# Performance work log

Measured on AMD Instinct MI355X. Metric: run time of the kernel, lower is better.

## Reference

```python
import jax, jax.numpy as jnp
import numpy as np

N, E, F_IN, H, C = 50000, 800000, 128, 64, 10

def setup_inputs() -> dict:
    key = jax.random.key(0)
    ks = jax.random.split(key, 8)
    x = jax.random.normal(ks[0], (N, F_IN), dtype=jnp.float32)
    edge_index = jax.random.randint(ks[1], (2, E), 0, N, dtype=jnp.int32)
    edge_weight = jax.random.uniform(ks[2], (E,), dtype=jnp.float32)
    W1 = jax.random.normal(ks[3], (H, F_IN), dtype=jnp.float32) * 0.05
    W2 = jax.random.normal(ks[4], (H, H), dtype=jnp.float32) * 0.05
    W3 = jax.random.normal(ks[5], (C, H), dtype=jnp.float32) * 0.05
    b1 = jnp.zeros((H,), jnp.float32)
    b2 = jnp.zeros((H,), jnp.float32)
    b3 = jnp.zeros((C,), jnp.float32)
    return {"x": x, "edge_index": edge_index, "edge_weight": edge_weight,
            "W1": W1, "b1": b1, "W2": W2, "b2": b2, "W3": W3, "b3": b3}

def reference(x, edge_index, edge_weight, W1, b1, W2, b2, W3, b3):
    n = x.shape[0]
    row, col = edge_index[0], edge_index[1]
    # GCN symmetric normalization (add_self_loops=False): deg from edge weights on col
    deg = jax.ops.segment_sum(edge_weight, col, num_segments=n)  # [N]
    dinv = jnp.where(deg > 0, jax.lax.rsqrt(deg), 0.0)
    norm = dinv[row] * edge_weight * dinv[col]  # [E]

    def gcn_layer(h, W, b):
        h = h @ W.T                               # linear transform [N, out]
        msg = h[row] * norm[:, None]              # gather + scale   [E, out]
        agg = jax.ops.segment_sum(msg, col, num_segments=n)  # scatter-add [N, out]
        return agg + b

    h = gcn_layer(x, W1, b1)
    h = gcn_layer(h, W2, b2)
    logits = gcn_layer(h, W3, b3)
    soft = jax.nn.softmax(logits, axis=1)
    return logits, soft
```

## Files before the change

### kernel.cpp

```cpp
#include <hip/hip_runtime.h>
#include <hip/hip_fp16.h>

#define N_NODES 50000
#define N_EDGES 800000
#define F_IN    128
#define H_DIM   64
#define C_DIM   10
#define CPAD    16
#define CAP     48
#define BLOCK   256
#define BIN_NODES 256
#define NBINS   196
#define STRIDE  4480
#define E_BLK   4096
#define ABLOCKS 196
#define DGB     (N_NODES / 16)
#define WB      ((N_NODES * 64) / 256)
#define POISON  ((int)0xAAAAAAAA)

__device__ __forceinline__ int unbase(int v) {
    return ((unsigned)v < 65536u) ? v : v - POISON;
}

__device__ __forceinline__ int   prow(unsigned v) { return (int)(v >> 16); }
__device__ __forceinline__ float pw(unsigned v)   {
    return __half2float(__ushort_as_half((unsigned short)(v & 0xFFFFu)));
}

__global__ __launch_bounds__(256) void k_binA(const int* __restrict__ rows,
                                              const int* __restrict__ cols,
                                              const float* __restrict__ ew,
                                              const float* __restrict__ W1,
                                              const float* __restrict__ b1,
                                              const float* __restrict__ W2,
                                              const float* __restrict__ b2,
                                              const float* __restrict__ W3,
                                              int* __restrict__ bucketCnt,
                                              unsigned* __restrict__ regionA,
                                              unsigned short* __restrict__ regionC,
                                              float* __restrict__ T2g,
                                              float* __restrict__ v1g,
                                              float* __restrict__ v2g) {
    const int tid = threadIdx.x;
    if (blockIdx.x < ABLOCKS) {
        __shared__ unsigned       sA[E_BLK];
        __shared__ unsigned short sC[E_BLK];
        __shared__ int hcnt[NBINS];
        __shared__ int lbase[NBINS];
        __shared__ int gb[NBINS];
        for (int i = tid; i < NBINS; i += BLOCK) hcnt[i] = 0;
        __syncthreads();

        const int e0 = blockIdx.x * E_BLK;
        unsigned rw[16];
        unsigned cl[16];
#pragma unroll
        for (int j = 0; j < 16; ++j) {
            int e = e0 + j * BLOCK + tid;
            if (e < N_EDGES) {
                int   c = cols[e];
                int   r = rows[e];
                float w = ew[e];
                rw[j] = ((unsigned)r << 16) | (unsigned)__half_as_ushort(__float2half(w));
                int lr = atomicAdd(&hcnt[c >> 8], 1);
                cl[j] = (unsigned)c | ((unsigned)lr << 16);
            } else {
                cl[j] = 0xFFFFFFFFu;
            }
        }
        __syncthreads();

        if (tid < 64) {
            int run = 0;
            for (int base = 0; base < NBINS; base += 64) {
                int i = base + tid;
                int v = (i < NBINS) ? hcnt[i] : 0;
                int s = v;
#pragma unroll
                for (int off = 1; off < 64; off <<= 1) {
                    int t = __shfl_up(s, off);
                    if (tid >= off) s += t;
                }
                if (i < NBINS) lbase[i] = run + s - v;
                run += __shfl(s, 63);
            }
        }
        __syncthreads();

#pragma unroll
        for (int j = 0; j < 16; ++j) {
            if (cl[j] != 0xFFFFFFFFu) {
                int c  = (int)(cl[j] & 0xFFFFu);
                int lr = (int)(cl[j] >> 16);
                int pos = lbase[c >> 8] + lr;
                sA[pos] = rw[j];
                sC[pos] = (unsigned short)c;
            }
        }
        if (tid < NBINS) gb[tid] = unbase(atomicAdd(&bucketCnt[tid], hcnt[tid]));
        __syncthreads();

        const int total = lbase[NBINS - 1] + hcnt[NBINS - 1];
        for (int i = tid; i < total; i += BLOCK) {
            int c = sC[i];
            int b = c >> 8;
            int gpos = gb[b] + (i - lbase[b]);
            if (gpos < STRIDE) {
                size_t p = (size_t)b * STRIDE + gpos;
                regionA[p] = sA[i];
                regionC[p] = (unsigned short)c;
            }
        }
        return;
    }

    __shared__ float u[C_DIM * H_DIM];
    for (int idx = tid; idx < C_DIM * H_DIM; idx += BLOCK) {
        int c = idx >> 6, j = idx & 63;
        float a = 0.f;
#pragma unroll
        for (int k = 0; k < H_DIM; ++k) a += W3[c * H_DIM + k] * W2[k * H_DIM + j];
        u[idx] = a;
    }
    __syncthreads();
    for (int idx = tid; idx < C_DIM * F_IN; idx += BLOCK) {
        int c = idx >> 7, f = idx & 127;
        float a = 0.f;
#pragma unroll
        for (int k = 0; k < H_DIM; ++k) a += u[c * H_DIM + k] * W1[k * F_IN + f];
        T2g[idx] = a;
    }
    if (tid < C_DIM) {
        float a = 0.f, b = 0.f;
#pragma unroll
        for (int k = 0; k < H_DIM; ++k) {
            a += u[tid * H_DIM + k] * b1[k];
            b += W3[tid * H_DIM + k] * b2[k];
        }
        v1g[tid] = a;
        v2g[tid] = b;
    }
}

__global__ __launch_bounds__(256) void k_binB(const int* __restrict__ bucketCnt,
                                              const unsigned* __restrict__ regionA,
                                              const unsigned short* __restrict__ regionC,
                                              int* __restrict__ cnt,
                                              float* __restrict__ dinv,
                                              unsigned* __restrict__ edata) {
    __shared__ unsigned sdata[BIN_NODES * CAP];
    __shared__ int   lcnt[BIN_NODES];
    __shared__ float wsum[BIN_NODES];
    const int tid = threadIdx.x;
    const int b   = blockIdx.x;
    if (tid < BIN_NODES) { lcnt[tid] = 0; wsum[tid] = 0.f; }
    __syncthreads();

    int tot = unbase(bucketCnt[b]);
    if (tot > STRIDE) tot = STRIDE;
    const size_t segBase = (size_t)b * STRIDE;
    for (int i = tid; i < tot; i += BLOCK) {
        unsigned e = regionA[segBase + i];
        int nl = (int)regionC[segBase + i] - b * BIN_NODES;
        int r = atomicAdd(&lcnt[nl], 1);
        if (r < CAP) sdata[nl * CAP + r] = e;
        atomicAdd(&wsum[nl], pw(e));
    }
    __syncthreads();

    const int n0 = b * BIN_NODES;
    const int nvalid = min(N_NODES - n0, BIN_NODES);
    int4* dst = reinterpret_cast<int4*>(edata + (size_t)n0 * CAP);
    const int4* src = reinterpret_cast<const int4*>(sdata);
    const int nvec = nvalid * CAP / 4;
    for (int i = tid; i < nvec; i += BLOCK) dst[i] = src[i];
    if (tid < nvalid) {
        int n = n0 + tid;
        cnt[n] = min(lcnt[tid], CAP);
        float d = wsum[tid];
        dinv[n] = d > 0.f ? rsqrtf(d) : 0.f;
    }
}

__global__ __launch_bounds__(256) void k_dg(const float* __restrict__ x,
                                            const float* __restrict__ T2g,
                                            const float* __restrict__ dinv,
                                            __half* __restrict__ bufA) {
    __shared__ float ts[16 * 132];
    __shared__ float xs[16][132];
    const int tid = threadIdx.x;
    const int n0 = blockIdx.x * 16;

    for (int i = tid; i < 16 * F_IN; i += BLOCK) {
        int c = i >> 7;
        ts[c * 132 + (i & 127)] = (c < C_DIM) ? T2g[i] : 0.f;
    }
    for (int i = tid; i < 16 * 32; i += BLOCK) {
        int ln = i >> 5, f4 = i & 31;
        float4 v = reinterpret_cast<const float4*>(x)[(n0 + ln) * 32 + f4];
        *reinterpret_cast<float4*>(&xs[ln][f4 * 4]) = v;
    }
    __syncthreads();

    const int g = tid >> 4;
    const int c = tid & 15;
    const int n = n0 + g;
    const float di = dinv[n];

    const float4* tsv = reinterpret_cast<const float4*>(&ts[c * 132]);
    const float4* xv  = reinterpret_cast<const float4*>(&xs[g][0]);
    float a = 0.f;
#pragma unroll 8
    for (int f4 = 0; f4 < 32; ++f4) {
        float4 xx = xv[f4], tt = tsv[f4];
        a += xx.x * tt.x + xx.y * tt.y + xx.z * tt.z + xx.w * tt.w;
    }
    float outv = (c < C_DIM) ? a * di : (c == 10 ? di : 0.f);
    bufA[n * CPAD + c] = __float2half(outv);
}

__global__ __launch_bounds__(256) void k_gather(const int* __restrict__ cnt,
                                                const unsigned* __restrict__ edata,
                                                const float* __restrict__ dinv,
                                                const __half* __restrict__ zin,
                                                __half* __restrict__ zout) {
    int n = (blockIdx.x * 256 + threadIdx.x) >> 6;
    if (n >= N_NODES) return;
    int lane = threadIdx.x & 63;
    int sub = lane >> 4, c = lane & 15;
    int count = cnt[n];
    if (count > CAP) count = CAP;
    int beg = n * CAP, end = beg + count;
    float acc = 0.f;
    int k = beg + sub;
    for (; k + 12 < end; k += 16) {
        unsigned e0 = edata[k];
        unsigned e1 = edata[k + 4];
        unsigned e2 = edata[k + 8];
        unsigned e3 = edata[k + 12];
        float v0 = __half2float(zin[prow(e0) * CPAD + c]);
        float v1 = __half2float(zin[prow(e1) * CPAD + c]);
        float v2 = __half2float(zin[prow(e2) * CPAD + c]);
        float v3 = __half2float(zin[prow(e3) * CPAD + c]);
        acc += pw(e0) * v0;
        acc += pw(e1) * v1;
        acc += pw(e2) * v2;
        acc += pw(e3) * v3;
    }
    for (; k < end; k += 4) {
        unsigned ed = edata[k];
        acc += pw(ed) * __half2float(zin[prow(ed) * CPAD + c]);
    }
    acc += __shfl_xor(acc, 32);
    acc += __shfl_xor(acc, 16);
    if (lane < 16) {
        float di = dinv[n];
        zout[n * CPAD + lane] = __float2half(acc * di * di);
    }
}

__global__ __launch_bounds__(256) void k_final(const int* __restrict__ cnt,
                                               const unsigned* __restrict__ edata,
                                               const float* __restrict__ dinv,
                                               const __half* __restrict__ zin,
                                               const __half* __restrict__ s1buf,
                                               const float* __restrict__ v1,
                                               const float* __restrict__ v2,
                                               const float* __restrict__ b3,
                                               float* __restrict__ logits,
                                               float* __restrict__ soft) {
    int n = (blockIdx.x * 256 + threadIdx.x) >> 6;
    if (n >= N_NODES) return;
    int lane = threadIdx.x & 63;
    int sub = lane >> 4, c = lane & 15;
    int count = cnt[n];
    if (count > CAP) count = CAP;
    int beg = n * CAP, end = beg + count;
    float acc = 0.f;
    int k = beg + sub;
    for (; k + 12 < end; k += 16) {
        unsigned e0 = edata[k];
        unsigned e1 = edata[k + 4];
        unsigned e2 = edata[k + 8];
        unsigned e3 = edata[k + 12];
        float w0 = __half2float(zin[prow(e0) * CPAD + c]);
        float w1 = __half2float(zin[prow(e1) * CPAD + c]);
        float w2 = __half2float(zin[prow(e2) * CPAD + c]);
        float w3 = __half2float(zin[prow(e3) * CPAD + c]);
        acc += pw(e0) * w0;
        acc += pw(e1) * w1;
        acc += pw(e2) * w2;
        acc += pw(e3) * w3;
    }
    for (; k < end; k += 4) {
        unsigned ed = edata[k];
        acc += pw(ed) * __half2float(zin[prow(ed) * CPAD + c]);
    }
    acc += __shfl_xor(acc, 32);
    acc += __shfl_xor(acc, 16);

    float di = dinv[n];
    float r  = di > 0.f ? 1.0f / di : 0.f;
    float a1 = __half2float(s1buf[n * CPAD + 10]) * r;
    float a2 = __half2float(zin[n * CPAD + 10]) * r;
    float l = (c < C_DIM) ? di * acc + a2 * v1[c] + a1 * v2[c] + b3[c] : -1e30f;
    float m = l;
#pragma unroll
    for (int d = 8; d >= 1; d >>= 1) m = fmaxf(m, __shfl_xor(m, d));
    float ev = (c < C_DIM) ? __expf(l - m) : 0.f;
    float s = ev;
#pragma unroll
    for (int d = 8; d >= 1; d >>= 1) s += __shfl_xor(s, d);
    if (lane < C_DIM) {
        logits[n * C_DIM + lane] = l;
        soft[n * C_DIM + lane]   = ev / s;
    }
}

extern "C" void kernel_launch(void* const* d_in, const int* in_sizes, int n_in,
                              void* d_out, int out_size, void* d_ws, size_t ws_size,
                              hipStream_t stream) {
    const float* x  = (const float*)d_in[0];
    const int*   ei = (const int*)d_in[1];
    const float* ew = (const float*)d_in[2];
    const float* W1 = (const float*)d_in[3];
    const float* b1 = (const float*)d_in[4];
    const float* W2 = (const float*)d_in[5];
    const float* b2 = (const float*)d_in[6];
    const float* W3 = (const float*)d_in[7];
    const float* b3 = (const float*)d_in[8];
    const int* rows = ei;
    const int* cols = ei + N_EDGES;

    char* ws = (char*)d_ws;
    size_t off = 0;
    auto alloc = [&](size_t bytes) { void* q = ws + off; off += (bytes + 15) & ~size_t(15); return q; };

    int*            cnt       = (int*)            alloc((size_t)N_NODES * 4);
    float*          dinv      = (float*)          alloc((size_t)N_NODES * 4);
    __half*         bufA      = (__half*)         alloc((size_t)N_NODES * CPAD * 2);
    __half*         bufB      = (__half*)         alloc((size_t)N_NODES * CPAD * 2);
    float*          T2g       = (float*)          alloc(C_DIM * F_IN * 4);
    float*          v1        = (float*)          alloc(64);
    float*          v2        = (float*)          alloc(64);
    int*            bucketCnt = (int*)            alloc(NBINS * 4);
    unsigned*       regionA   = (unsigned*)       alloc((size_t)NBINS * STRIDE * 4);
    unsigned short* regionC   = (unsigned short*) alloc((size_t)NBINS * STRIDE * 2);
    unsigned*       edata     = (unsigned*)       alloc((size_t)N_NODES * CAP * 4);

    float* logits = (float*)d_out;
    float* soft   = logits + N_NODES * C_DIM;

    k_binA<<<ABLOCKS + 1, 256, 0, stream>>>(rows, cols, ew, W1, b1, W2, b2, W3,
                                            bucketCnt, regionA, regionC, T2g, v1, v2);
    k_binB<<<NBINS, 256, 0, stream>>>(bucketCnt, regionA, regionC, cnt, dinv, edata);
    k_dg<<<DGB, 256, 0, stream>>>(x, T2g, dinv, bufA);
    k_gather<<<WB, 256, 0, stream>>>(cnt, edata, dinv, bufA, bufB);
    k_gather<<<WB, 256, 0, stream>>>(cnt, edata, dinv, bufB, bufA);
    k_final<<<WB, 256, 0, stream>>>(cnt, edata, dinv, bufA, bufB, v1, v2, b3,
                                    logits, soft);
}
```

Baseline: 177.8 us.

## Pack dinv and padded count into float2 meta, zero-pad edge lists, halve binning block

Per-node dinv and edge count are merged into one float2 array so each gather thread makes a single metadata load. Edge lists are zero-padded to a multiple of 16 inside binB, which lets the gather and final kernels run a fixed unrolled loop of up to 3 iterations with no tail loop. The binning kernel now covers 2048 edges per block, doubling the block count and halving per-thread register arrays. In exchange, padded zero-weight entries gather row 0, adding wasted loads, and binB gains an extra sync.

New measurement: 166.7 us. 6.2% less time.

```diff
diff --git a/kernel.cpp b/kernel.cpp
--- a/kernel.cpp
+++ b/kernel.cpp
@@ -12,8 +12,8 @@
 #define BIN_NODES 256
 #define NBINS   196
 #define STRIDE  4480
-#define E_BLK   4096
-#define ABLOCKS 196
+#define E_BLK   2048
+#define ABLOCKS ((N_EDGES + E_BLK - 1) / E_BLK)
 #define DGB     (N_NODES / 16)
 #define WB      ((N_NODES * 64) / 256)
 #define POISON  ((int)0xAAAAAAAA)
@@ -52,10 +52,10 @@
         __syncthreads();
 
         const int e0 = blockIdx.x * E_BLK;
-        unsigned rw[16];
-        unsigned cl[16];
-#pragma unroll
-        for (int j = 0; j < 16; ++j) {
+        unsigned rw[8];
+        unsigned cl[8];
+#pragma unroll
+        for (int j = 0; j < 8; ++j) {
             int e = e0 + j * BLOCK + tid;
             if (e < N_EDGES) {
                 int   c = cols[e];
@@ -88,7 +88,7 @@
         __syncthreads();
 
 #pragma unroll
-        for (int j = 0; j < 16; ++j) {
+        for (int j = 0; j < 8; ++j) {
             if (cl[j] != 0xFFFFFFFFu) {
                 int c  = (int)(cl[j] & 0xFFFFu);
                 int lr = (int)(cl[j] >> 16);
@@ -145,8 +145,7 @@
 __global__ __launch_bounds__(256) void k_binB(const int* __restrict__ bucketCnt,
                                               const unsigned* __restrict__ regionA,
                                               const unsigned short* __restrict__ regionC,
-                                              int* __restrict__ cnt,
-                                              float* __restrict__ dinv,
+                                              float2* __restrict__ meta,
                                               unsigned* __restrict__ edata) {
     __shared__ unsigned sdata[BIN_NODES * CAP];
     __shared__ int   lcnt[BIN_NODES];
@@ -170,21 +169,25 @@
 
     const int n0 = b * BIN_NODES;
     const int nvalid = min(N_NODES - n0, BIN_NODES);
+    if (tid < nvalid) {
+        int c0 = min(lcnt[tid], CAP);
+        int cp = (c0 + 15) & ~15;
+        if (cp > CAP) cp = CAP;
+        for (int r = c0; r < cp; ++r) sdata[tid * CAP + r] = 0u;
+        float d = wsum[tid];
+        meta[n0 + tid] = make_float2(d > 0.f ? rsqrtf(d) : 0.f, (float)cp);
+    }
+    __syncthreads();
+
     int4* dst = reinterpret_cast<int4*>(edata + (size_t)n0 * CAP);
     const int4* src = reinterpret_cast<const int4*>(sdata);
     const int nvec = nvalid * CAP / 4;
     for (int i = tid; i < nvec; i += BLOCK) dst[i] = src[i];
-    if (tid < nvalid) {
-        int n = n0 + tid;
-        cnt[n] = min(lcnt[tid], CAP);
-        float d = wsum[tid];
-        dinv[n] = d > 0.f ? rsqrtf(d) : 0.f;
-    }
 }
 
 __global__ __launch_bounds__(256) void k_dg(const float* __restrict__ x,
                                             const float* __restrict__ T2g,
-                                            const float* __restrict__ dinv,
+                                            const float2* __restrict__ meta,
                                             __half* __restrict__ bufA) {
     __shared__ float ts[16 * 132];
     __shared__ float xs[16][132];
@@ -205,7 +208,7 @@
     const int g = tid >> 4;
     const int c = tid & 15;
     const int n = n0 + g;
-    const float di = dinv[n];
+    const float di = meta[n].x;
 
     const float4* tsv = reinterpret_cast<const float4*>(&ts[c * 132]);
     const float4* xv  = reinterpret_cast<const float4*>(&xs[g][0]);
@@ -219,49 +222,40 @@
     bufA[n * CPAD + c] = __float2half(outv);
 }
 
-__global__ __launch_bounds__(256) void k_gather(const int* __restrict__ cnt,
+__global__ __launch_bounds__(256) void k_gather(const float2* __restrict__ meta,
                                                 const unsigned* __restrict__ edata,
-                                                const float* __restrict__ dinv,
                                                 const __half* __restrict__ zin,
                                                 __half* __restrict__ zout) {
     int n = (blockIdx.x * 256 + threadIdx.x) >> 6;
     if (n >= N_NODES) return;
     int lane = threadIdx.x & 63;
     int sub = lane >> 4, c = lane & 15;
-    int count = cnt[n];
-    if (count > CAP) count = CAP;
-    int beg = n * CAP, end = beg + count;
+    float2 m = meta[n];
+    float di = m.x;
+    int iters = ((int)m.y) >> 4;
+    int base = n * CAP + sub;
     float acc = 0.f;
-    int k = beg + sub;
-    for (; k + 12 < end; k += 16) {
-        unsigned e0 = edata[k];
-        unsigned e1 = edata[k + 4];
-        unsigned e2 = edata[k + 8];
-        unsigned e3 = edata[k + 12];
-        float v0 = __half2float(zin[prow(e0) * CPAD + c]);
-        float v1 = __half2float(zin[prow(e1) * CPAD + c]);
-        float v2 = __half2float(zin[prow(e2) * CPAD + c]);
-        float v3 = __half2float(zin[prow(e3) * CPAD + c]);
-        acc += pw(e0) * v0;
-        acc += pw(e1) * v1;
-        acc += pw(e2) * v2;
-        acc += pw(e3) * v3;
-    }
-    for (; k < end; k += 4) {
-        unsigned ed = edata[k];
-        acc += pw(ed) * __half2float(zin[prow(ed) * CPAD + c]);
+#pragma unroll
+    for (int i = 0; i < 3; ++i) {
+        if (i < iters) {
+            int k = base + i * 16;
+            unsigned e0 = edata[k];
+            unsigned e1 = edata[k + 4];
+            unsigned e2 = edata[k + 8];
+            unsigned e3 = edata[k + 12];
+            acc += pw(e0) * __half2float(zin[prow(e0) * CPAD + c]);
+            acc += pw(e1) * __half2float(zin[prow(e1) * CPAD + c]);
+            acc += pw(e2) * __half2float(zin[prow(e2) * CPAD + c]);
+            acc += pw(e3) * __half2float(zin[prow(e3) * CPAD + c]);
+        }
     }
     acc += __shfl_xor(acc, 32);
     acc += __shfl_xor(acc, 16);
-    if (lane < 16) {
-        float di = dinv[n];
-        zout[n * CPAD + lane] = __float2half(acc * di * di);
-    }
-}
-
-__global__ __launch_bounds__(256) void k_final(const int* __restrict__ cnt,
+    if (lane < 16) zout[n * CPAD + lane] = __float2half(acc * di * di);
+}
+
+__global__ __launch_bounds__(256) void k_final(const float2* __restrict__ meta,
                                                const unsigned* __restrict__ edata,
-                                               const float* __restrict__ dinv,
                                                const __half* __restrict__ zin,
                                                const __half* __restrict__ s1buf,
                                                const float* __restrict__ v1,
@@ -273,41 +267,36 @@
     if (n >= N_NODES) return;
     int lane = threadIdx.x & 63;
     int sub = lane >> 4, c = lane & 15;
-    int count = cnt[n];
-    if (count > CAP) count = CAP;
-    int beg = n * CAP, end = beg + count;
+    float2 m = meta[n];
+    float di = m.x;
+    int iters = ((int)m.y) >> 4;
+    int base = n * CAP + sub;
     float acc = 0.f;
-    int k = beg + sub;
-    for (; k + 12 < end; k += 16) {
-        unsigned e0 = edata[k];
-        unsigned e1 = edata[k + 4];
-        unsigned e2 = edata[k + 8];
-        unsigned e3 = edata[k + 12];
-        float w0 = __half2float(zin[prow(e0) * CPAD + c]);
-        float w1 = __half2float(zin[prow(e1) * CPAD + c]);
-        float w2 = __half2float(zin[prow(e2) * CPAD + c]);
-        float w3 = __half2float(zin[prow(e3) * CPAD + c]);
-        acc += pw(e0) * w0;
-        acc += pw(e1) * w1;
-        acc += pw(e2) * w2;
-        acc += pw(e3) * w3;
-    }
-    for (; k < end; k += 4) {
-        unsigned ed = edata[k];
-        acc += pw(ed) * __half2float(zin[prow(ed) * CPAD + c]);
+#pragma unroll
+    for (int i = 0; i < 3; ++i) {
+        if (i < iters) {
+            int k = base + i * 16;
+            unsigned e0 = edata[k];
+            unsigned e1 = edata[k + 4];
+            unsigned e2 = edata[k + 8];
+            unsigned e3 = edata[k + 12];
+            acc += pw(e0) * __half2float(zin[prow(e0) * CPAD + c]);
+            acc += pw(e1) * __half2float(zin[prow(e1) * CPAD + c]);
+            acc += pw(e2) * __half2float(zin[prow(e2) * CPAD + c]);
+            acc += pw(e3) * __half2float(zin[prow(e3) * CPAD + c]);
+        }
     }
     acc += __shfl_xor(acc, 32);
     acc += __shfl_xor(acc, 16);
 
-    float di = dinv[n];
     float r  = di > 0.f ? 1.0f / di : 0.f;
     float a1 = __half2float(s1buf[n * CPAD + 10]) * r;
     float a2 = __half2float(zin[n * CPAD + 10]) * r;
     float l = (c < C_DIM) ? di * acc + a2 * v1[c] + a1 * v2[c] + b3[c] : -1e30f;
-    float m = l;
-#pragma unroll
-    for (int d = 8; d >= 1; d >>= 1) m = fmaxf(m, __shfl_xor(m, d));
-    float ev = (c < C_DIM) ? __expf(l - m) : 0.f;
+    float mx = l;
+#pragma unroll
+    for (int d = 8; d >= 1; d >>= 1) mx = fmaxf(mx, __shfl_xor(mx, d));
+    float ev = (c < C_DIM) ? __expf(l - mx) : 0.f;
     float s = ev;
 #pragma unroll
     for (int d = 8; d >= 1; d >>= 1) s += __shfl_xor(s, d);
@@ -336,8 +325,7 @@
     size_t off = 0;
     auto alloc = [&](size_t bytes) { void* q = ws + off; off += (bytes + 15) & ~size_t(15); return q; };
 
-    int*            cnt       = (int*)            alloc((size_t)N_NODES * 4);
-    float*          dinv      = (float*)          alloc((size_t)N_NODES * 4);
+    float2*         meta      = (float2*)         alloc((size_t)N_NODES * 8);
     __half*         bufA      = (__half*)         alloc((size_t)N_NODES * CPAD * 2);
     __half*         bufB      = (__half*)         alloc((size_t)N_NODES * CPAD * 2);
     float*          T2g       = (float*)          alloc(C_DIM * F_IN * 4);
@@ -353,10 +341,10 @@
 
     k_binA<<<ABLOCKS + 1, 256, 0, stream>>>(rows, cols, ew, W1, b1, W2, b2, W3,
                                             bucketCnt, regionA, regionC, T2g, v1, v2);
-    k_binB<<<NBINS, 256, 0, stream>>>(bucketCnt, regionA, regionC, cnt, dinv, edata);
-    k_dg<<<DGB, 256, 0, stream>>>(x, T2g, dinv, bufA);
-    k_gather<<<WB, 256, 0, stream>>>(cnt, edata, dinv, bufA, bufB);
-    k_gather<<<WB, 256, 0, stream>>>(cnt, edata, dinv, bufB, bufA);
-    k_final<<<WB, 256, 0, stream>>>(cnt, edata, dinv, bufA, bufB, v1, v2, b3,
+    k_binB<<<NBINS, 256, 0, stream>>>(bucketCnt, regionA, regionC, meta, edata);
+    k_dg<<<DGB, 256, 0, stream>>>(x, T2g, meta, bufA);
+    k_gather<<<WB, 256, 0, stream>>>(meta, edata, bufA, bufB);
+    k_gather<<<WB, 256, 0, stream>>>(meta, edata, bufB, bufA);
+    k_final<<<WB, 256, 0, stream>>>(meta, edata, bufA, bufB, v1, v2, b3,
                                     logits, soft);
 }
```
